# Kernel optimization log

Hardware: AMD Instinct MI355X
Metric: run time of the kernel (lower is better)

Reference implementation:

```python
import jax, jax.numpy as jnp
import numpy as np

N_NODES = 100000
N_EDGES = 800000
C = 64        # in_channels == out_channels
H = 4         # num_heads
LN_EPS = 1e-5
SM_EPS = 1e-8


def setup_inputs() -> dict:
    key = jax.random.key(0)
    ks = jax.random.split(key, 8)
    return {
        "x": jax.random.normal(ks[0], (N_NODES, C), dtype=jnp.float32),
        "edge_index": jax.random.randint(ks[1], (2, N_EDGES), 0, N_NODES, dtype=jnp.int64),
        "edge_time": jax.random.uniform(ks[2], (N_EDGES,), dtype=jnp.float32),
        "current_time": 1,
        "W_w": jax.random.normal(ks[3], (C, C), dtype=jnp.float32) * (1.0 / np.sqrt(C)),
        "W_b": jnp.zeros((C,), dtype=jnp.float32),
        "attn_w": jax.random.normal(ks[4], (2 * C, H), dtype=jnp.float32) * (1.0 / np.sqrt(2 * C)),
        "attn_b": jnp.zeros((H,), dtype=jnp.float32),
        "decay_rate": jnp.full((1,), 0.1, dtype=jnp.float32),
        "proj_w": jax.random.normal(ks[5], (C * H, C), dtype=jnp.float32) * (1.0 / np.sqrt(C * H)),
        "proj_b": jnp.zeros((C,), dtype=jnp.float32),
        "ln_g": jnp.ones((C,), dtype=jnp.float32),
        "ln_b": jnp.zeros((C,), dtype=jnp.float32),
    }


def reference(x, edge_index, edge_time, current_time, W_w, W_b, attn_w, attn_b,
              decay_rate, proj_w, proj_b, ln_g, ln_b):
    num_nodes = x.shape[0]
    src, dst = edge_index[0], edge_index[1]

    # relation-specific transform (same Linear applied to src and dst node sets)
    h = x @ W_w + W_b                       # (N, C)
    h_src = h[src]                          # (E, C) gather
    h_dst = h[dst]                          # (E, C) gather

    # attention: Linear(2C -> H) + LeakyReLU(0.2)
    logits = h_src @ attn_w[:C] + h_dst @ attn_w[C:] + attn_b   # (E, H)
    scores = jax.nn.leaky_relu(logits, negative_slope=0.2)

    # temporal decay: exp(-softplus(lambda) * delta_t), multiplied pre-softmax
    delta_t = jnp.float32(current_time) - edge_time             # (E,)
    lam = jax.nn.softplus(decay_rate[0])
    scores = scores * jnp.exp(-lam * delta_t)[:, None]

    # segmented (per-destination) softmax over incoming edges
    smax = jax.ops.segment_max(scores, dst, num_segments=num_nodes)   # (N, H)
    e = jnp.exp(scores - smax[dst])                                   # (E, H)
    ssum = jax.ops.segment_sum(e, dst, num_segments=num_nodes)        # (N, H)
    attn = e / (ssum[dst] + SM_EPS)                                   # (E, H)

    # per-edge messages (E, C, H) -> (E, C*H), scatter-add to destinations
    msg = (h_src[:, :, None] * attn[:, None, :]).reshape(-1, C * H)
    agg = jax.ops.segment_sum(msg, dst, num_segments=num_nodes)       # (N, C*H)

    # single edge type -> mean over 1 message is identity
    out = agg @ proj_w + proj_b                                       # (N, C)
    # dropout p=0 (eval) -> identity; residual + LayerNorm + ReLU
    z = out + x
    mu = jnp.mean(z, axis=-1, keepdims=True)
    var = jnp.mean(jnp.square(z - mu), axis=-1, keepdims=True)
    y = ln_g * (z - mu) * jax.lax.rsqrt(var + LN_EPS) + ln_b
    return jax.nn.relu(y)
```

## Files before the change

kernel.cpp:

```cpp
#include <hip/hip_runtime.h>


typedef __attribute__((ext_vector_type(8))) short bf16x8;
typedef __attribute__((ext_vector_type(4))) float f32x4;

__device__ __forceinline__ unsigned short f2bf(float f) {
  unsigned int u = __float_as_uint(f);
  u += 0x7FFFu + ((u >> 16) & 1u);
  return (unsigned short)(u >> 16);
}
__device__ __forceinline__ float bf2f(unsigned short s) {
  return __uint_as_float(((unsigned int)s) << 16);
}
__device__ __forceinline__ unsigned int pk(float a, float b) {
  return (unsigned int)f2bf(a) | ((unsigned int)f2bf(b) << 16);
}
__device__ __forceinline__ float bflo(int u) {
  return __uint_as_float(((unsigned int)u) << 16);
}
__device__ __forceinline__ float bfhi(int u) {
  return __uint_as_float(((unsigned int)u) & 0xFFFF0000u);
}

#define FMA4(P, S, R) { P.x = fmaf(S, R.x, P.x); P.y = fmaf(S, R.y, P.y); \
                        P.z = fmaf(S, R.z, P.z); P.w = fmaf(S, R.w, P.w); }

__global__ __launch_bounds__(256) void k_init(const float* __restrict__ Pw,
    unsigned short* __restrict__ Bf, int* __restrict__ deg, int N)
{
  int i = blockIdx.x * 256 + threadIdx.x;
  if (i < N) deg[i] = 0;
  if (i < 16384) {
    int j    = i & 7;
    int lane = (i >> 3) & 63;
    int cb   = (i >> 9) & 3;
    int ks   = i >> 11;
    int k    = ks * 32 + (lane >> 4) * 8 + j;
    int colg = cb * 16 + (lane & 15);
    Bf[i] = f2bf(Pw[(size_t)k * 64 + colg]);
  }
}

__global__ __launch_bounds__(256, 2) void k_hd(const float* __restrict__ x,
    const float* __restrict__ Ww, const float* __restrict__ Wb,
    const float* __restrict__ attn_w, const int* __restrict__ ei,
    unsigned short* __restrict__ h16, float4* __restrict__ u,
    float4* __restrict__ v, int* __restrict__ deg, int* __restrict__ rank,
    int N, int E, int NBn)
{
  if ((int)blockIdx.x >= NBn) {
    int e = (blockIdx.x - NBn) * 256 + threadIdx.x;
    if (e < E) rank[e] = atomicAdd(&deg[ei[E + e]], 1);
    return;
  }
  const int n = blockIdx.x * 256 + threadIdx.x;
  const bool valid = (n < N);
  const int nc = valid ? n : (N - 1);

  float o[64];
  #pragma unroll
  for (int c = 0; c < 64; ++c) o[c] = Wb[c];

  const float* xr = x + (size_t)nc * 64;
  for (int ch = 0; ch < 16; ++ch) {
    float4 xv = *(const float4*)(xr + ch * 4);
    float a[4] = {xv.x, xv.y, xv.z, xv.w};
    #pragma unroll
    for (int kk = 0; kk < 4; ++kk) {
      const float* Wr = Ww + (size_t)(ch * 4 + kk) * 64;
      #pragma unroll
      for (int c = 0; c < 64; ++c)
        o[c] = fmaf(a[kk], Wr[c], o[c]);
    }
  }

  float4 uu = make_float4(0.f, 0.f, 0.f, 0.f);
  float4 vv = make_float4(0.f, 0.f, 0.f, 0.f);
  const float4* aw = (const float4*)attn_w;
  #pragma unroll
  for (int c = 0; c < 64; ++c) {
    float4 r1 = aw[c];
    float4 r2 = aw[64 + c];
    FMA4(uu, o[c], r1);
    FMA4(vv, o[c], r2);
  }

  if (valid) {
    unsigned int* hr = (unsigned int*)(h16 + (size_t)n * 64);
    #pragma unroll
    for (int i = 0; i < 8; ++i) {
      uint4 w;
      w.x = pk(o[i*8+0], o[i*8+1]);
      w.y = pk(o[i*8+2], o[i*8+3]);
      w.z = pk(o[i*8+4], o[i*8+5]);
      w.w = pk(o[i*8+6], o[i*8+7]);
      *(uint4*)(hr + i * 4) = w;
    }
    u[n] = uu;
    v[n] = vv;
  }
}

__global__ __launch_bounds__(256) void scan1(const int* __restrict__ deg,
    int* __restrict__ offs, int* __restrict__ bsums, int N)
{
  int i = blockIdx.x * 256 + threadIdx.x;
  int lane = threadIdx.x & 63;
  int w = threadIdx.x >> 6;
  int v = (i < N) ? deg[i] : 0;
  int s = v;
  #pragma unroll
  for (int d = 1; d < 64; d <<= 1) {
    int t = __shfl_up(s, d, 64);
    if (lane >= d) s += t;
  }
  __shared__ int wsum[4];
  if (lane == 63) wsum[w] = s;
  __syncthreads();
  int add = 0;
  if (w > 0) add += wsum[0];
  if (w > 1) add += wsum[1];
  if (w > 2) add += wsum[2];
  if (i < N) offs[i] = s - v + add;
  if (threadIdx.x == 255) bsums[blockIdx.x] = wsum[0] + wsum[1] + wsum[2] + wsum[3];
}

__global__ __launch_bounds__(512) void scan2(int* bsums, int NB)
{
  __shared__ int lds[512];
  int t = threadIdx.x;
  int v = (t < NB) ? bsums[t] : 0;
  lds[t] = v;
  __syncthreads();
  for (int s = 1; s < 512; s <<= 1) {
    int a = (t >= s) ? lds[t - s] : 0;
    __syncthreads();
    lds[t] += a;
    __syncthreads();
  }
  if (t < NB) bsums[t] = lds[t] - v;
}

__global__ __launch_bounds__(256) void k_fill(const int* __restrict__ ei,
    const float* __restrict__ et, const int* __restrict__ ctime,
    const float* __restrict__ drate, const float4* __restrict__ u,
    const float4* __restrict__ v, const float* __restrict__ attn_b,
    const int* __restrict__ offs, const int* __restrict__ bsums,
    const int* __restrict__ rank, int4* __restrict__ csr, int E)
{
  int e = blockIdx.x * 256 + threadIdx.x;
  if (e >= E) return;
  const int s = ei[e];
  const int d = ei[E + e];
  const float4 us = u[s];
  const float4 vd = v[d];
  const float4 ab = *(const float4*)attn_b;
  const float lam = log1pf(__expf(drate[0]));
  const float w = __expf(-lam * ((float)ctime[0] - et[e]));

  float4 o; float t;
  t = us.x + vd.x + ab.x; t = (t > 0.f ? t : 0.2f * t) * w; o.x = __expf(t);
  t = us.y + vd.y + ab.y; t = (t > 0.f ? t : 0.2f * t) * w; o.y = __expf(t);
  t = us.z + vd.z + ab.z; t = (t > 0.f ? t : 0.2f * t) * w; o.z = __expf(t);
  t = us.w + vd.w + ab.w; t = (t > 0.f ? t : 0.2f * t) * w; o.w = __expf(t);

  int4 rec;
  rec.x = s;
  rec.y = (int)pk(o.x, o.y);
  rec.z = (int)pk(o.z, o.w);
  rec.w = 0;
  csr[offs[d] + bsums[d >> 8] + rank[e]] = rec;
}

__global__ __launch_bounds__(256) void k_agg(const unsigned short* __restrict__ h16,
    const int4* __restrict__ csr, const int* __restrict__ offs,
    const int* __restrict__ bsums, unsigned short* __restrict__ agg,
    int N, int E)
{
  const int c = threadIdx.x & 63;
  const int wid = blockIdx.x * 4 + (threadIdx.x >> 6);
  const int wstride = gridDim.x * 4;

  for (int n0 = wid; n0 < N; n0 += wstride) {
    const int n = __builtin_amdgcn_readfirstlane(n0);
    const int p0 = offs[n] + bsums[n >> 8];
    const int p1 = (n + 1 < N) ? (offs[n + 1] + bsums[(n + 1) >> 8]) : E;
    const int nf = (p1 - p0) & ~3;

    float acc0 = 0.f, acc1 = 0.f, acc2 = 0.f, acc3 = 0.f;
    float den0 = 0.f, den1 = 0.f, den2 = 0.f, den3 = 0.f;

    int4 rA0, rA1, rA2, rA3;
    float gA0 = 0.f, gA1 = 0.f, gA2 = 0.f, gA3 = 0.f;
    if (nf) {
      rA0 = csr[p0];     rA1 = csr[p0 + 1];
      rA2 = csr[p0 + 2]; rA3 = csr[p0 + 3];
      gA0 = bf2f(h16[(size_t)rA0.x * 64 + c]);
      gA1 = bf2f(h16[(size_t)rA1.x * 64 + c]);
      gA2 = bf2f(h16[(size_t)rA2.x * 64 + c]);
      gA3 = bf2f(h16[(size_t)rA3.x * 64 + c]);
    }
    for (int p = p0; p < p0 + nf; p += 4) {
      int4 rB0, rB1, rB2, rB3;
      float gB0, gB1, gB2, gB3;
      const bool more = (p + 4 < p0 + nf);
      if (more) {
        rB0 = csr[p + 4]; rB1 = csr[p + 5];
        rB2 = csr[p + 6]; rB3 = csr[p + 7];
        gB0 = bf2f(h16[(size_t)rB0.x * 64 + c]);
        gB1 = bf2f(h16[(size_t)rB1.x * 64 + c]);
        gB2 = bf2f(h16[(size_t)rB2.x * 64 + c]);
        gB3 = bf2f(h16[(size_t)rB3.x * 64 + c]);
      }
      float e00 = bflo(rA0.y), e01 = bfhi(rA0.y), e02 = bflo(rA0.z), e03 = bfhi(rA0.z);
      float e10 = bflo(rA1.y), e11 = bfhi(rA1.y), e12 = bflo(rA1.z), e13 = bfhi(rA1.z);
      float e20 = bflo(rA2.y), e21 = bfhi(rA2.y), e22 = bflo(rA2.z), e23 = bfhi(rA2.z);
      float e30 = bflo(rA3.y), e31 = bfhi(rA3.y), e32 = bflo(rA3.z), e33 = bfhi(rA3.z);
      den0 += (e00 + e10) + (e20 + e30);
      den1 += (e01 + e11) + (e21 + e31);
      den2 += (e02 + e12) + (e22 + e32);
      den3 += (e03 + e13) + (e23 + e33);
      acc0 = fmaf(e00, gA0, fmaf(e10, gA1, fmaf(e20, gA2, fmaf(e30, gA3, acc0))));
      acc1 = fmaf(e01, gA0, fmaf(e11, gA1, fmaf(e21, gA2, fmaf(e31, gA3, acc1))));
      acc2 = fmaf(e02, gA0, fmaf(e12, gA1, fmaf(e22, gA2, fmaf(e32, gA3, acc2))));
      acc3 = fmaf(e03, gA0, fmaf(e13, gA1, fmaf(e23, gA2, fmaf(e33, gA3, acc3))));
      if (more) {
        rA0 = rB0; rA1 = rB1; rA2 = rB2; rA3 = rB3;
        gA0 = gB0; gA1 = gB1; gA2 = gB2; gA3 = gB3;
      }
    }
    for (int p = p0 + nf; p < p1; ++p) {
      int4 r = csr[p];
      float g = bf2f(h16[(size_t)r.x * 64 + c]);
      float e0 = bflo(r.y), e1 = bfhi(r.y), e2 = bflo(r.z), e3 = bfhi(r.z);
      den0 += e0; den1 += e1; den2 += e2; den3 += e3;
      acc0 = fmaf(e0, g, acc0);
      acc1 = fmaf(e1, g, acc1);
      acc2 = fmaf(e2, g, acc2);
      acc3 = fmaf(e3, g, acc3);
    }
    uint2 w;
    w.x = pk(acc0 / (den0 + 1e-8f), acc1 / (den1 + 1e-8f));
    w.y = pk(acc2 / (den2 + 1e-8f), acc3 / (den3 + 1e-8f));
    *(uint2*)(agg + (size_t)n * 256 + c * 4) = w;
  }
}

__global__ __launch_bounds__(256) void k_projm(const unsigned short* __restrict__ agg,
    const unsigned short* __restrict__ Bf, const float* __restrict__ x,
    const float* __restrict__ Pb,
    const float* __restrict__ lg, const float* __restrict__ lb,
    float* __restrict__ out, int N)
{
  const int lane = threadIdx.x & 63;
  const int wv = threadIdx.x >> 6;
  const int nt = blockIdx.x * 4 + wv;
  if (nt * 16 >= N) return;
  const int col  = lane & 15;
  const int quad = lane >> 4;
  const int base = nt * 16;

  int na = base + col; if (na >= N) na = N - 1;
  const unsigned short* aptr = agg + (size_t)na * 256 + quad * 8;

  f32x4 acc0 = {0.f, 0.f, 0.f, 0.f};
  f32x4 acc1 = {0.f, 0.f, 0.f, 0.f};
  f32x4 acc2 = {0.f, 0.f, 0.f, 0.f};
  f32x4 acc3 = {0.f, 0.f, 0.f, 0.f};

  #pragma unroll
  for (int ks = 0; ks < 8; ++ks) {
    bf16x8 av = *(const bf16x8*)(aptr + ks * 32);
    bf16x8 b0 = *(const bf16x8*)(Bf + ((size_t)(ks * 4 + 0) * 64 + lane) * 8);
    bf16x8 b1 = *(const bf16x8*)(Bf + ((size_t)(ks * 4 + 1) * 64 + lane) * 8);
    bf16x8 b2 = *(const bf16x8*)(Bf + ((size_t)(ks * 4 + 2) * 64 + lane) * 8);
    bf16x8 b3 = *(const bf16x8*)(Bf + ((size_t)(ks * 4 + 3) * 64 + lane) * 8);
    acc0 = __builtin_amdgcn_mfma_f32_16x16x32_bf16(av, b0, acc0, 0, 0, 0);
    acc1 = __builtin_amdgcn_mfma_f32_16x16x32_bf16(av, b1, acc1, 0, 0, 0);
    acc2 = __builtin_amdgcn_mfma_f32_16x16x32_bf16(av, b2, acc2, 0, 0, 0);
    acc3 = __builtin_amdgcn_mfma_f32_16x16x32_bf16(av, b3, acc3, 0, 0, 0);
  }

  const float pb0 = Pb[col], pb1 = Pb[16 + col], pb2 = Pb[32 + col], pb3 = Pb[48 + col];
  float v[4][4];
  #pragma unroll
  for (int r = 0; r < 4; ++r) {
    int node = base + quad * 4 + r; if (node >= N) node = N - 1;
    const float* xr = x + (size_t)node * 64;
    v[0][r] = acc0[r] + pb0 + xr[col];
    v[1][r] = acc1[r] + pb1 + xr[16 + col];
    v[2][r] = acc2[r] + pb2 + xr[32 + col];
    v[3][r] = acc3[r] + pb3 + xr[48 + col];
  }

  float mu[4], inv[4];
  #pragma unroll
  for (int r = 0; r < 4; ++r) {
    float s = (v[0][r] + v[1][r]) + (v[2][r] + v[3][r]);
    s += __shfl_xor(s, 1, 64); s += __shfl_xor(s, 2, 64);
    s += __shfl_xor(s, 4, 64); s += __shfl_xor(s, 8, 64);
    mu[r] = s * 0.015625f;
  }
  #pragma unroll
  for (int r = 0; r < 4; ++r) {
    float d0 = v[0][r] - mu[r], d1 = v[1][r] - mu[r];
    float d2 = v[2][r] - mu[r], d3 = v[3][r] - mu[r];
    float s = fmaf(d0, d0, d1 * d1) + fmaf(d2, d2, d3 * d3);
    s += __shfl_xor(s, 1, 64); s += __shfl_xor(s, 2, 64);
    s += __shfl_xor(s, 4, 64); s += __shfl_xor(s, 8, 64);
    inv[r] = rsqrtf(s * 0.015625f + 1e-5f);
  }

  const float lg0 = lg[col], lg1 = lg[16 + col], lg2 = lg[32 + col], lg3 = lg[48 + col];
  const float lb0 = lb[col], lb1 = lb[16 + col], lb2 = lb[32 + col], lb3 = lb[48 + col];
  #pragma unroll
  for (int r = 0; r < 4; ++r) {
    int node = base + quad * 4 + r;
    if (node < N) {
      float* orow = out + (size_t)node * 64;
      orow[col]      = fmaxf(fmaf(lg0 * (v[0][r] - mu[r]), inv[r], lb0), 0.f);
      orow[16 + col] = fmaxf(fmaf(lg1 * (v[1][r] - mu[r]), inv[r], lb1), 0.f);
      orow[32 + col] = fmaxf(fmaf(lg2 * (v[2][r] - mu[r]), inv[r], lb2), 0.f);
      orow[48 + col] = fmaxf(fmaf(lg3 * (v[3][r] - mu[r]), inv[r], lb3), 0.f);
    }
  }
}

extern "C" void kernel_launch(void* const* d_in, const int* in_sizes, int n_in,
                              void* d_out, int out_size, void* d_ws, size_t ws_size,
                              hipStream_t stream)
{
  const float* x  = (const float*)d_in[0];
  const int*   ei = (const int*)d_in[1];
  const float* et = (const float*)d_in[2];
  const int*   ct = (const int*)d_in[3];
  const float* Ww = (const float*)d_in[4];
  const float* Wb = (const float*)d_in[5];
  const float* aw = (const float*)d_in[6];
  const float* ab = (const float*)d_in[7];
  const float* dr = (const float*)d_in[8];
  const float* Pw = (const float*)d_in[9];
  const float* Pb = (const float*)d_in[10];
  const float* lg = (const float*)d_in[11];
  const float* lb = (const float*)d_in[12];
  float* out = (float*)d_out;

  const int N = in_sizes[0] / 64;
  const int E = in_sizes[2];

  char* ws = (char*)d_ws;
  size_t off = 0;
  auto take = [&](size_t bytes) -> char* {
    char* p = ws + off;
    off = (off + bytes + 255) & ~(size_t)255;
    return p;
  };
  unsigned short* h16 = (unsigned short*)take((size_t)N * 64 * 2);
  int*    deg    = (int*)take((size_t)N * 4);
  int*    offs   = (int*)take((size_t)N * 4);
  int*    bsums  = (int*)take(512 * 4);
  int*    rank   = (int*)take((size_t)E * 4);
  int4*   csr    = (int4*)take((size_t)E * 16);
  unsigned short* agg = (unsigned short*)take((size_t)N * 256 * 2);
  float4* u      = (float4*)take((size_t)N * 16);
  float4* v      = (float4*)take((size_t)N * 16);
  unsigned short* Bf = (unsigned short*)take(16384 * 2);

  const int NBn = (N + 255) / 256;
  const int NBe = (E + 255) / 256;

  k_init<<<NBn, 256, 0, stream>>>(Pw, Bf, deg, N);
  k_hd<<<NBn + NBe, 256, 0, stream>>>(x, Ww, Wb, aw, ei, h16, u, v, deg, rank, N, E, NBn);
  scan1<<<NBn, 256, 0, stream>>>(deg, offs, bsums, N);
  scan2<<<1, 512, 0, stream>>>(bsums, NBn);
  k_fill<<<NBe, 256, 0, stream>>>(ei, et, ct, dr, u, v, ab, offs, bsums, rank, csr, E);
  k_agg<<<2048, 256, 0, stream>>>(h16, csr, offs, bsums, agg, N, E);
  const int NT = (N + 15) / 16;
  k_projm<<<(NT + 3) / 4, 256, 0, stream>>>(agg, Bf, x, Pb, lg, lb, out, N);
}
```

Baseline: 252.0 us.

## Compute node linear transform with split-bf16 MFMA instead of scalar FMA

Replaces the per-thread scalar 64x64 FP32 matmul in the node-transform kernel with wave-level 16x16x32 bf16 MFMA. Both x and W are split into hi and lo bf16 parts and three MFMAs are summed to approximate FP32 accuracy. The attention projections u and v are now computed by cross-lane shuffle reductions. This is meant to remove the register-heavy, ALU-bound scalar loop, at the cost of a small precision loss and narrow 2-byte strided stores to h16.

New measurement: 249.4 us. No clear change (-1.0%).

```diff
diff --git a/kernel.cpp b/kernel.cpp
--- a/kernel.cpp
+++ b/kernel.cpp
@@ -26,7 +26,9 @@
                         P.z = fmaf(S, R.z, P.z); P.w = fmaf(S, R.w, P.w); }
 
 __global__ __launch_bounds__(256) void k_init(const float* __restrict__ Pw,
-    unsigned short* __restrict__ Bf, int* __restrict__ deg, int N)
+    const float* __restrict__ Ww, unsigned short* __restrict__ Bf,
+    unsigned short* __restrict__ Whi, unsigned short* __restrict__ Wlo,
+    int* __restrict__ deg, int N)
 {
   int i = blockIdx.x * 256 + threadIdx.x;
   if (i < N) deg[i] = 0;
@@ -39,11 +41,24 @@
     int colg = cb * 16 + (lane & 15);
     Bf[i] = f2bf(Pw[(size_t)k * 64 + colg]);
   }
-}
-
-__global__ __launch_bounds__(256, 2) void k_hd(const float* __restrict__ x,
-    const float* __restrict__ Ww, const float* __restrict__ Wb,
-    const float* __restrict__ attn_w, const int* __restrict__ ei,
+  if (i < 4096) {
+    int j    = i & 7;
+    int lane = (i >> 3) & 63;
+    int cb   = (i >> 9) & 3;
+    int ks   = i >> 11;
+    int k    = ks * 32 + (lane >> 4) * 8 + j;
+    int colg = cb * 16 + (lane & 15);
+    float w = Ww[(size_t)k * 64 + colg];
+    unsigned short hi = f2bf(w);
+    Whi[i] = hi;
+    Wlo[i] = f2bf(w - bf2f(hi));
+  }
+}
+
+__global__ __launch_bounds__(256) void k_hm(const float* __restrict__ x,
+    const unsigned short* __restrict__ Whi, const unsigned short* __restrict__ Wlo,
+    const float* __restrict__ Wb, const float* __restrict__ attn_w,
+    const int* __restrict__ ei,
     unsigned short* __restrict__ h16, float4* __restrict__ u,
     float4* __restrict__ v, int* __restrict__ deg, int* __restrict__ rank,
     int N, int E, int NBn)
@@ -53,51 +68,83 @@
     if (e < E) rank[e] = atomicAdd(&deg[ei[E + e]], 1);
     return;
   }
-  const int n = blockIdx.x * 256 + threadIdx.x;
-  const bool valid = (n < N);
-  const int nc = valid ? n : (N - 1);
-
-  float o[64];
-  #pragma unroll
-  for (int c = 0; c < 64; ++c) o[c] = Wb[c];
-
-  const float* xr = x + (size_t)nc * 64;
-  for (int ch = 0; ch < 16; ++ch) {
-    float4 xv = *(const float4*)(xr + ch * 4);
-    float a[4] = {xv.x, xv.y, xv.z, xv.w};
+  const int lane = threadIdx.x & 63;
+  const int wv = threadIdx.x >> 6;
+  const int nt = blockIdx.x * 4 + wv;
+  if (nt * 16 >= N) return;
+  const int col  = lane & 15;
+  const int quad = lane >> 4;
+  const int base = nt * 16;
+
+  int na = base + col; if (na >= N) na = N - 1;
+
+  f32x4 acc0 = {0.f, 0.f, 0.f, 0.f};
+  f32x4 acc1 = {0.f, 0.f, 0.f, 0.f};
+  f32x4 acc2 = {0.f, 0.f, 0.f, 0.f};
+  f32x4 acc3 = {0.f, 0.f, 0.f, 0.f};
+
+  #pragma unroll
+  for (int ks = 0; ks < 2; ++ks) {
+    const float* xr = x + (size_t)na * 64 + ks * 32 + quad * 8;
+    float4 xa = *(const float4*)xr;
+    float4 xb = *(const float4*)(xr + 4);
+    float xv[8] = {xa.x, xa.y, xa.z, xa.w, xb.x, xb.y, xb.z, xb.w};
+    bf16x8 ah, al;
     #pragma unroll
-    for (int kk = 0; kk < 4; ++kk) {
-      const float* Wr = Ww + (size_t)(ch * 4 + kk) * 64;
-      #pragma unroll
-      for (int c = 0; c < 64; ++c)
-        o[c] = fmaf(a[kk], Wr[c], o[c]);
-    }
-  }
-
-  float4 uu = make_float4(0.f, 0.f, 0.f, 0.f);
-  float4 vv = make_float4(0.f, 0.f, 0.f, 0.f);
+    for (int j = 0; j < 8; ++j) {
+      unsigned short hi = f2bf(xv[j]);
+      ah[j] = (short)hi;
+      al[j] = (short)f2bf(xv[j] - bf2f(hi));
+    }
+    #pragma unroll
+    for (int cb = 0; cb < 4; ++cb) {
+      const size_t bo = ((size_t)(ks * 4 + cb) * 64 + lane) * 8;
+      bf16x8 bh = *(const bf16x8*)(Whi + bo);
+      bf16x8 bl = *(const bf16x8*)(Wlo + bo);
+      f32x4 a = (cb == 0) ? acc0 : (cb == 1) ? acc1 : (cb == 2) ? acc2 : acc3;
+      a = __builtin_amdgcn_mfma_f32_16x16x32_bf16(ah, bh, a, 0, 0, 0);
+      a = __builtin_amdgcn_mfma_f32_16x16x32_bf16(ah, bl, a, 0, 0, 0);
+      a = __builtin_amdgcn_mfma_f32_16x16x32_bf16(al, bh, a, 0, 0, 0);
+      if (cb == 0) acc0 = a; else if (cb == 1) acc1 = a;
+      else if (cb == 2) acc2 = a; else acc3 = a;
+    }
+  }
+
+  const float wb0 = Wb[col], wb1 = Wb[16 + col], wb2 = Wb[32 + col], wb3 = Wb[48 + col];
   const float4* aw = (const float4*)attn_w;
-  #pragma unroll
-  for (int c = 0; c < 64; ++c) {
-    float4 r1 = aw[c];
-    float4 r2 = aw[64 + c];
-    FMA4(uu, o[c], r1);
-    FMA4(vv, o[c], r2);
-  }
-
-  if (valid) {
-    unsigned int* hr = (unsigned int*)(h16 + (size_t)n * 64);
+  const float4 a10 = aw[col],      a11 = aw[16 + col],
+               a12 = aw[32 + col], a13 = aw[48 + col];
+  const float4 a20 = aw[64 + col],      a21 = aw[80 + col],
+               a22 = aw[96 + col],      a23 = aw[112 + col];
+
+  #pragma unroll
+  for (int r = 0; r < 4; ++r) {
+    const int node = base + quad * 4 + r;
+    float h0 = acc0[r] + wb0;
+    float h1 = acc1[r] + wb1;
+    float h2 = acc2[r] + wb2;
+    float h3 = acc3[r] + wb3;
+
+    if (node < N) {
+      unsigned short* hrow = h16 + (size_t)node * 64;
+      hrow[col]      = f2bf(h0);
+      hrow[16 + col] = f2bf(h1);
+      hrow[32 + col] = f2bf(h2);
+      hrow[48 + col] = f2bf(h3);
+    }
+
+    float4 up = make_float4(0.f, 0.f, 0.f, 0.f);
+    float4 vp = make_float4(0.f, 0.f, 0.f, 0.f);
+    FMA4(up, h0, a10); FMA4(up, h1, a11); FMA4(up, h2, a12); FMA4(up, h3, a13);
+    FMA4(vp, h0, a20); FMA4(vp, h1, a21); FMA4(vp, h2, a22); FMA4(vp, h3, a23);
     #pragma unroll
-    for (int i = 0; i < 8; ++i) {
-      uint4 w;
-      w.x = pk(o[i*8+0], o[i*8+1]);
-      w.y = pk(o[i*8+2], o[i*8+3]);
-      w.z = pk(o[i*8+4], o[i*8+5]);
-      w.w = pk(o[i*8+6], o[i*8+7]);
-      *(uint4*)(hr + i * 4) = w;
-    }
-    u[n] = uu;
-    v[n] = vv;
+    for (int m = 1; m < 16; m <<= 1) {
+      up.x += __shfl_xor(up.x, m, 64); up.y += __shfl_xor(up.y, m, 64);
+      up.z += __shfl_xor(up.z, m, 64); up.w += __shfl_xor(up.w, m, 64);
+      vp.x += __shfl_xor(vp.x, m, 64); vp.y += __shfl_xor(vp.y, m, 64);
+      vp.z += __shfl_xor(vp.z, m, 64); vp.w += __shfl_xor(vp.w, m, 64);
+    }
+    if (col == 0 && node < N) { u[node] = up; v[node] = vp; }
   }
 }
 
@@ -364,13 +411,17 @@
   unsigned short* agg = (unsigned short*)take((size_t)N * 256 * 2);
   float4* u      = (float4*)take((size_t)N * 16);
   float4* v      = (float4*)take((size_t)N * 16);
-  unsigned short* Bf = (unsigned short*)take(16384 * 2);
+  unsigned short* Bf  = (unsigned short*)take(16384 * 2);
+  unsigned short* Whi = (unsigned short*)take(4096 * 2);
+  unsigned short* Wlo = (unsigned short*)take(4096 * 2);
 
   const int NBn = (N + 255) / 256;
   const int NBe = (E + 255) / 256;
-
-  k_init<<<NBn, 256, 0, stream>>>(Pw, Bf, deg, N);
-  k_hd<<<NBn + NBe, 256, 0, stream>>>(x, Ww, Wb, aw, ei, h16, u, v, deg, rank, N, E, NBn);
+  const int NBt = (N + 63) / 64;
+
+  k_init<<<NBn, 256, 0, stream>>>(Pw, Ww, Bf, Whi, Wlo, deg, N);
+  k_hm<<<NBt + NBe, 256, 0, stream>>>(x, Whi, Wlo, Wb, aw, ei, h16, u, v,
+                                      deg, rank, N, E, NBt);
   scan1<<<NBn, 256, 0, stream>>>(deg, offs, bsums, N);
   scan2<<<1, 512, 0, stream>>>(bsums, NBn);
   k_fill<<<NBe, 256, 0, stream>>>(ei, et, ct, dr, u, v, ab, offs, bsums, rank, csr, E);
```
